# Optimization experiments

Hardware: AMD Instinct MI355X
Metric: run time of the kernel (lower is better)

The kernel has to match this reference:

```python
import jax, jax.numpy as jnp
import numpy as np


def setup_inputs() -> dict:
    key = jax.random.key(0)
    ks = jax.random.split(key, 9)
    B, T, C = 4, 2048, 2048
    E, I, SI = 8, 1408, 5632
    s = lambda k, shape, fan_in: jax.random.normal(k, shape, jnp.float32) * (fan_in ** -0.5)
    return {
        "x": jax.random.normal(ks[0], (B, T, C), jnp.float32),
        "gate_w": s(ks[1], (C, E), C),                  # router: x @ gate_w -> [N,E]
        "expert_gate_w": s(ks[2], (E, C, I), C),        # stacked gate_proj weights
        "expert_up_w": s(ks[3], (E, C, I), C),          # stacked up_proj weights
        "expert_down_w": s(ks[4], (E, I, C), I),        # stacked down_proj weights
        "shared_gate_w": s(ks[5], (C, SI), C),
        "shared_up_w": s(ks[6], (C, SI), C),
        "shared_down_w": s(ks[7], (SI, C), SI),
        "shared_expert_gate_w": s(ks[8], (C, 1), C),
        "top_k": 4,
    }


def reference(x, gate_w, expert_gate_w, expert_up_w, expert_down_w,
              shared_gate_w, shared_up_w, shared_down_w, shared_expert_gate_w, top_k):
    B, T, C = x.shape
    E = gate_w.shape[1]
    xf = x.reshape(-1, C)                      # [N, C]
    N = xf.shape[0]

    # --- router: softmax (fp32) -> top-k -> renormalize ---
    logits = xf @ gate_w                       # [N, E]
    probs = jax.nn.softmax(logits.astype(jnp.float32), axis=-1)
    w, idx = jax.lax.top_k(probs, top_k)       # [N, k]
    w = w / jnp.sum(w, axis=-1, keepdims=True)

    # dense combine gates [N, E]: zero for non-selected experts (equivalent to
    # the torch dispatch/sort/combine: each token gets weight w_k on expert idx_k)
    gates = jnp.zeros((N, E), jnp.float32).at[jnp.arange(N)[:, None], idx].add(w)

    # --- per-expert SwiGLU MLP, accumulated via scan over experts ---
    def step(acc, ew):
        wg, wu, wd, g = ew                     # wg/wu: [C,I], wd: [I,C], g: [N]
        h = jax.nn.silu(xf @ wg) * (xf @ wu)   # [N, I]
        return acc + g[:, None] * (h @ wd), None

    routed, _ = jax.lax.scan(
        step, jnp.zeros_like(xf),
        (expert_gate_w, expert_up_w, expert_down_w, gates.T))

    # --- shared expert with sigmoid gate ---
    shared = (jax.nn.silu(xf @ shared_gate_w) * (xf @ shared_up_w)) @ shared_down_w
    sg = jax.nn.sigmoid(xf @ shared_expert_gate_w)   # [N, 1]

    return (routed + sg * shared).reshape(B, T, C)
```

## Files before the change

kernel.cpp:

```cpp
#include <hip/hip_runtime.h>
#include <hip/hip_bf16.h>
#include <stdint.h>


typedef float f32x4 __attribute__((ext_vector_type(4)));
typedef int   i32x4 __attribute__((ext_vector_type(4)));
typedef __hip_bfloat16 bf16;

#define DEV __device__ __forceinline__

DEV void mfma16(f32x4& c, const i32x4& a, const i32x4& b) {
    asm("v_mfma_f32_16x16x32_bf16 %0, %1, %2, %0" : "+v"(c) : "v"(a), "v"(b));
}

template<int ROWS>
DEV void stage(const bf16* gtile, long ldK, char* lds, int tid) {
    const int wid = tid >> 6, lane = tid & 63;
    const int swz = ((lane & 7) ^ (lane >> 3)) << 4;
    constexpr int NISS = (ROWS * 128) / 4096;
    #pragma unroll
    for (int i = 0; i < NISS; i++) {
        const int o = i * 4096 + wid * 1024;
        const int row = (o >> 7) + (lane >> 3);
        const char* ga = (const char*)gtile + (long)row * (ldK * 2) + swz;
        __builtin_amdgcn_global_load_lds(
            (const __attribute__((address_space(1))) void*)ga,
            (__attribute__((address_space(3))) void*)(lds + o), 16, 0, 0);
    }
}

template<int ROWS>
DEV void stage_idx(const char* base, const long* roff, int ktb, char* lds,
                   int tid, int swz) {
    const int wid = tid >> 6;
    constexpr int NISS = (ROWS * 128) / 4096;
    #pragma unroll
    for (int i = 0; i < NISS; i++) {
        const int o = i * 4096 + wid * 1024;
        const char* ga = base + roff[i] + ktb + swz;
        __builtin_amdgcn_global_load_lds(
            (const __attribute__((address_space(1))) void*)ga,
            (__attribute__((address_space(3))) void*)(lds + o), 16, 0, 0);
    }
}

DEV i32x4 ldsfrag(const char* lds, int row, int kbyte) {
    const int off = (row << 7) + (kbyte ^ ((row & 7) << 4));
    return *(const i32x4*)(lds + off);
}

__global__ __launch_bounds__(256) void tcvt(const float* __restrict__ srcA,
        bf16* __restrict__ dstA, const float* __restrict__ srcB,
        bf16* __restrict__ dstB, int Cd, long dld, long sz, long dz,
        int zsplit) {
    __shared__ float t[64][65];
    long z = blockIdx.z;
    const float* src; bf16* dst;
    if ((int)z < zsplit) { src = srcA; dst = dstA; }
    else { src = srcB; dst = dstB; z -= zsplit; }
    src += z * sz; dst += z * dz;
    const int cb = blockIdx.x * 64, rb = blockIdx.y * 64;
    const int tx = threadIdx.x & 63, ty = threadIdx.x >> 6;
    #pragma unroll
    for (int i = 0; i < 16; i++) {
        const int r = ty + i * 4;
        t[r][tx] = src[(long)(rb + r) * Cd + cb + tx];
    }
    __syncthreads();
    #pragma unroll
    for (int i = 0; i < 16; i++) {
        const int c = ty + i * 4;
        dst[(long)(cb + c) * dld + rb + tx] = __float2bfloat16(t[tx][c]);
    }
}

__global__ __launch_bounds__(256) void cvtx(const float* __restrict__ x,
        bf16* __restrict__ xb, long n4) {
    long i = (long)blockIdx.x * blockDim.x + threadIdx.x;
    const long stride = (long)gridDim.x * blockDim.x;
    for (; i < n4; i += stride) {
        const float4 v = ((const float4*)x)[i];
        union { bf16 h[4]; ushort4 u; } cu;
        cu.h[0] = __float2bfloat16(v.x); cu.h[1] = __float2bfloat16(v.y);
        cu.h[2] = __float2bfloat16(v.z); cu.h[3] = __float2bfloat16(v.w);
        ((ushort4*)xb)[i] = cu.u;
    }
}

__global__ __launch_bounds__(256) void router(const float* __restrict__ x,
        const float* __restrict__ gw, const float* __restrict__ segw,
        int* __restrict__ tidx, float* __restrict__ tw,
        float* __restrict__ sg, int C) {
    const int lane = threadIdx.x & 63;
    const long t = (long)blockIdx.x * 4 + (threadIdx.x >> 6);
    const float* xr = x + t * C;
    float a[9];
    #pragma unroll
    for (int e = 0; e < 9; e++) a[e] = 0.f;
    for (int c = lane; c < C; c += 64) {
        const float xv = xr[c];
        const float4* g4 = (const float4*)(gw + (long)c * 8);
        const float4 g0 = g4[0], g1 = g4[1];
        a[0] += xv * g0.x; a[1] += xv * g0.y; a[2] += xv * g0.z; a[3] += xv * g0.w;
        a[4] += xv * g1.x; a[5] += xv * g1.y; a[6] += xv * g1.z; a[7] += xv * g1.w;
        a[8] += xv * segw[c];
    }
    #pragma unroll
    for (int e = 0; e < 9; e++) {
        #pragma unroll
        for (int o = 32; o; o >>= 1) a[e] += __shfl_xor(a[e], o, 64);
    }
    if (lane == 0) {
        float m = a[0];
        #pragma unroll
        for (int e = 1; e < 8; e++) m = fmaxf(m, a[e]);
        float p[8]; float s = 0.f;
        #pragma unroll
        for (int e = 0; e < 8; e++) { p[e] = expf(a[e] - m); s += p[e]; }
        #pragma unroll
        for (int e = 0; e < 8; e++) p[e] /= s;
        bool used[8] = {false,false,false,false,false,false,false,false};
        float wsum = 0.f; int idx[4]; float wv[4];
        for (int k = 0; k < 4; k++) {
            float best = -1.f; int bi = 0;
            for (int e = 0; e < 8; e++)
                if (!used[e] && p[e] > best) { best = p[e]; bi = e; }
            used[bi] = true; idx[k] = bi; wv[k] = best; wsum += best;
        }
        int4 iv; float4 wv4;
        iv.x = idx[0]; iv.y = idx[1]; iv.z = idx[2]; iv.w = idx[3];
        wv4.x = wv[0] / wsum; wv4.y = wv[1] / wsum;
        wv4.z = wv[2] / wsum; wv4.w = wv[3] / wsum;
        ((int4*)tidx)[t] = iv;
        ((float4*)tw)[t] = wv4;
        sg[t] = 1.f / (1.f + expf(-a[8]));
    }
}

__global__ __launch_bounds__(256) void build_lists(const int* __restrict__ tidx,
        const float* __restrict__ tw, int* __restrict__ tok,
        float* __restrict__ wl, int* __restrict__ cnt, int N) {
    const int e = blockIdx.x;
    const int tid = threadIdx.x;
    const int per = N / 256;
    __shared__ int csum[256];
    int c = 0;
    for (int i = 0; i < per; i++) {
        const int4 id4 = ((const int4*)tidx)[tid * per + i];
        if (id4.x == e || id4.y == e || id4.z == e || id4.w == e) c++;
    }
    csum[tid] = c;
    __syncthreads();
    for (int o = 1; o < 256; o <<= 1) {
        const int v = (tid >= o) ? csum[tid - o] : 0;
        __syncthreads();
        csum[tid] += v;
        __syncthreads();
    }
    int pos = csum[tid] - c;
    if (tid == 255) cnt[e] = csum[255];
    for (int i = 0; i < per; i++) {
        const int t = tid * per + i;
        const int4   id4 = ((const int4*)tidx)[t];
        const float4 w4  = ((const float4*)tw)[t];
        float w = 0.f; int hit = 0;
        if      (id4.x == e) { w = w4.x; hit = 1; }
        else if (id4.y == e) { w = w4.y; hit = 1; }
        else if (id4.z == e) { w = w4.z; hit = 1; }
        else if (id4.w == e) { w = w4.w; hit = 1; }
        if (hit) { tok[(long)e * N + pos] = t; wl[(long)e * N + pos] = w; pos++; }
    }
}

template<int TAG>
__global__ __launch_bounds__(256) void dual_gemm_t(const bf16* __restrict__ A,
        const int* __restrict__ tok, long tokz,
        const int* __restrict__ cnt, int Mfix,
        const bf16* __restrict__ BG0, const bf16* __restrict__ BU0, long bz,
        bf16* __restrict__ H0, long hld, long hz,
        const float* __restrict__ sc0, long scz, int K) {
    __shared__ __align__(128) char Al[16384];
    __shared__ __align__(128) char Gl[8192];
    __shared__ __align__(128) char Ul[8192];
    const int z = blockIdx.z;
    const int Me = cnt ? cnt[z] : Mfix;
    const long m0 = (long)blockIdx.x * 128;
    if (m0 >= Me) return;
    const int* ridx = tok ? tok + (long)z * tokz : nullptr;
    const bf16* BG = BG0 + (long)z * bz;
    const bf16* BU = BU0 + (long)z * bz;
    bf16* H = H0 + (long)z * hz;
    const float* sc = sc0 + (long)z * scz;
    const int tid = threadIdx.x, lane = tid & 63, wid = tid >> 6;
    const long n0 = (long)blockIdx.y * 64;
    const int wm = (wid >> 1) * 64, wn = (wid & 1) * 32;
    const int l15 = lane & 15, lhi = lane >> 4;
    const int swz = ((lane & 7) ^ (lane >> 3)) << 4;
    long roffA[4];
    #pragma unroll
    for (int i = 0; i < 4; i++) {
        const int rit = ((i * 4096 + wid * 1024) >> 7) + (lane >> 3);
        int g = (int)m0 + rit;
        if (ridx) g = ridx[g < Me ? g : Me - 1];
        roffA[i] = (long)g * (K * 2);
    }
    f32x4 ag[4][2] = {}; f32x4 au[4][2] = {};
    for (int kt = 0; kt < K; kt += 64) {
        stage_idx<128>((const char*)A, roffA, kt * 2, Al, tid, swz);
        stage<64>(BG + n0 * K + kt, (long)K, Gl, tid);
        stage<64>(BU + n0 * K + kt, (long)K, Ul, tid);
        __syncthreads();
        #pragma unroll
        for (int ks = 0; ks < 2; ks++) {
            const int kb = ks * 64 + lhi * 16;
            i32x4 af[4], bg[2], bu[2];
            #pragma unroll
            for (int mi = 0; mi < 4; mi++) af[mi] = ldsfrag(Al, wm + mi * 16 + l15, kb);
            #pragma unroll
            for (int ni = 0; ni < 2; ni++) {
                bg[ni] = ldsfrag(Gl, wn + ni * 16 + l15, kb);
                bu[ni] = ldsfrag(Ul, wn + ni * 16 + l15, kb);
            }
            #pragma unroll
            for (int mi = 0; mi < 4; mi++) {
                #pragma unroll
                for (int ni = 0; ni < 2; ni++) {
                    mfma16(ag[mi][ni], af[mi], bg[ni]);
                    mfma16(au[mi][ni], af[mi], bu[ni]);
                }
            }
        }
        __syncthreads();
    }
    asm volatile("s_nop 7\n\ts_nop 7\n\ts_nop 7");
    #pragma unroll
    for (int mi = 0; mi < 4; mi++) {
        #pragma unroll
        for (int r = 0; r < 4; r++) {
            const int pos = (int)m0 + wm + mi * 16 + lhi * 4 + r;
            if (pos < Me) {
                const float s = sc[pos];
                #pragma unroll
                for (int ni = 0; ni < 2; ni++) {
                    const float gv = ag[mi][ni][r], uv = au[mi][ni][r];
                    const float h = (gv / (1.f + expf(-gv))) * uv * s;
                    H[(long)pos * hld + n0 + wn + ni * 16 + l15] = __float2bfloat16(h);
                }
            }
        }
    }
}

template<int TAG>
__global__ __launch_bounds__(256) void gemm_down_t(const bf16* __restrict__ A,
        const bf16* __restrict__ BT, float* __restrict__ C,
        const int* __restrict__ ridx, const int* __restrict__ cntp, int Mfix,
        int K, long ldc, int beta) {
    __shared__ __align__(128) char Al[16384];
    __shared__ __align__(128) char Bl[16384];
    const int Me = cntp ? *cntp : Mfix;
    const long m0 = (long)blockIdx.y * 128;
    if (m0 >= Me) return;
    const int tid = threadIdx.x, lane = tid & 63, wid = tid >> 6;
    const long n0 = (long)blockIdx.x * 128;
    const int wm = (wid >> 1) * 64, wn = (wid & 1) * 64;
    const int l15 = lane & 15, lhi = lane >> 4;
    f32x4 acc[4][4] = {};
    for (int kt = 0; kt < K; kt += 64) {
        stage<128>(A  + m0 * K + kt, (long)K, Al, tid);
        stage<128>(BT + n0 * K + kt, (long)K, Bl, tid);
        __syncthreads();
        #pragma unroll
        for (int ks = 0; ks < 2; ks++) {
            const int kb = ks * 64 + lhi * 16;
            i32x4 af[4], bfr[4];
            #pragma unroll
            for (int mi = 0; mi < 4; mi++) af[mi]  = ldsfrag(Al, wm + mi * 16 + l15, kb);
            #pragma unroll
            for (int ni = 0; ni < 4; ni++) bfr[ni] = ldsfrag(Bl, wn + ni * 16 + l15, kb);
            #pragma unroll
            for (int mi = 0; mi < 4; mi++) {
                #pragma unroll
                for (int ni = 0; ni < 4; ni++) mfma16(acc[mi][ni], af[mi], bfr[ni]);
            }
        }
        __syncthreads();
    }
    asm volatile("s_nop 7\n\ts_nop 7\n\ts_nop 7");
    #pragma unroll
    for (int mi = 0; mi < 4; mi++) {
        #pragma unroll
        for (int r = 0; r < 4; r++) {
            const int pos = (int)m0 + wm + mi * 16 + lhi * 4 + r;
            if (pos < Me) {
                const long orow = ridx ? (long)ridx[pos] : (long)pos;
                #pragma unroll
                for (int ni = 0; ni < 4; ni++) {
                    const long ci = orow * ldc + n0 + wn + ni * 16 + l15;
                    float v = acc[mi][ni][r];
                    if (beta) v += C[ci];
                    C[ci] = v;
                }
            }
        }
    }
}

extern "C" void kernel_launch(void* const* d_in, const int* in_sizes, int n_in,
                              void* d_out, int out_size, void* d_ws, size_t ws_size,
                              hipStream_t stream) {
    const int N = 8192, Cdim = 2048, E = 8, I = 1408, SI = 5632;

    const float* x    = (const float*)d_in[0];
    const float* gw   = (const float*)d_in[1];
    const float* egw  = (const float*)d_in[2];
    const float* euw  = (const float*)d_in[3];
    const float* edw  = (const float*)d_in[4];
    const float* sgw  = (const float*)d_in[5];
    const float* suw  = (const float*)d_in[6];
    const float* sdw  = (const float*)d_in[7];
    const float* segw = (const float*)d_in[8];
    float* out = (float*)d_out;

    char* ws = (char*)d_ws;
    size_t off = 0;
    auto alloc = [&](size_t bytes) { char* p = ws + off; off += (bytes + 255) & ~(size_t)255; return p; };

    bf16*  xb   = (bf16*) alloc((size_t)N * Cdim * 2);
    int*   tidx = (int*)  alloc((size_t)N * 4 * 4);
    float* tw   = (float*)alloc((size_t)N * 4 * 4);
    float* sg   = (float*)alloc((size_t)N * 4);
    int*   tok  = (int*)  alloc((size_t)E * N * 4);
    float* wl   = (float*)alloc((size_t)E * N * 4);
    int*   cnt  = (int*)  alloc(256);
    const size_t commonEnd = off;

    auto planNeed = [&](int EB) {
        const size_t slot = (size_t)(EB * I > SI ? EB * I : SI) * Cdim * 2;
        const size_t h    = (size_t)N * (EB * I > SI ? (size_t)EB * I : (size_t)SI) * 2;
        return commonEnd + 3 * slot + h + 4096;
    };
    const int EB = (ws_size >= planNeed(8)) ? 8 : 4;
    const size_t WSLOT = (size_t)(EB * I > SI ? EB * I : SI) * Cdim * 2;
    const size_t HROWS = (size_t)(EB * I > SI ? (size_t)EB * I : (size_t)SI);
    bf16* Wa = (bf16*)alloc(WSLOT);
    bf16* Wb = (bf16*)alloc(WSLOT);
    bf16* Wc = (bf16*)alloc(WSLOT);
    bf16* Hc = (bf16*)alloc((size_t)N * HROWS * 2);
    if (off > ws_size) return;

    cvtx<<<4096, 256, 0, stream>>>(x, xb, (long)N * Cdim / 4);
    router<<<N / 4, 256, 0, stream>>>(x, gw, segw, tidx, tw, sg, Cdim);
    build_lists<<<E, 256, 0, stream>>>(tidx, tw, tok, wl, cnt, N);

    tcvt<<<dim3(SI / 64, Cdim / 64, 2), 256, 0, stream>>>(
            sgw, Wa, suw, Wb, SI, (long)Cdim, 0, 0, 1);
    tcvt<<<dim3(Cdim / 64, SI / 64, 1), 256, 0, stream>>>(
            sdw, Wc, nullptr, nullptr, Cdim, (long)SI, 0, 0, 1);
    dual_gemm_t<0><<<dim3(N / 128, SI / 64, 1), 256, 0, stream>>>(xb,
            nullptr, 0, nullptr, N, Wa, Wb, 0, Hc, (long)SI, 0, sg, 0, Cdim);
    gemm_down_t<0><<<dim3(Cdim / 128, N / 128), 256, 0, stream>>>(Hc, Wc, out,
            nullptr, nullptr, N, SI, (long)Cdim, 0);

    for (int b = 0; b < E / EB; b++) {
        const int e0 = b * EB;
        tcvt<<<dim3(I / 64, Cdim / 64, 2 * EB), 256, 0, stream>>>(
                egw + (long)e0 * Cdim * I, Wa, euw + (long)e0 * Cdim * I, Wb,
                I, (long)Cdim, (long)Cdim * I, (long)I * Cdim, EB);
        tcvt<<<dim3(Cdim / 64, I / 64, EB), 256, 0, stream>>>(
                edw + (long)e0 * I * Cdim, Wc, nullptr, nullptr,
                Cdim, (long)I, (long)I * Cdim, (long)Cdim * I, EB);

        dual_gemm_t<1><<<dim3(N / 128, I / 64, EB), 256, 0, stream>>>(xb,
                tok + (long)e0 * N, (long)N, cnt + e0, 0,
                Wa, Wb, (long)I * Cdim,
                Hc, (long)I, (long)N * I,
                wl + (long)e0 * N, (long)N, Cdim);

        for (int z = 0; z < EB; z++) {
            gemm_down_t<1><<<dim3(Cdim / 128, N / 128), 256, 0, stream>>>(
                    Hc + (long)z * N * I, Wc + (long)z * Cdim * I, out,
                    tok + (long)(e0 + z) * N, cnt + e0 + z, 0,
                    I, (long)Cdim, 1);
        }
    }
}
```

Before: 1.610 ms.

## Merge shared and routed expert gate/up GEMMs into one launch with compact H

Fuses the x-to-bf16 conversion into the router kernel. Adds a prefix scan over per-expert token counts so the routed hidden activations are stored compactly (4N rows) instead of as N rows per expert. Merges the shared-expert and all routed-expert gate/up GEMMs into one grid launch, so the shared expert fills the tail of the unevenly sized expert work. The aim is fewer launches, less idle GPU time between kernels, less workspace traffic, and a single read of x. The cost is a larger workspace and a heterogeneous grid with branchy per-block setup.

Measured after the change: 1.576 ms. 2.1% less time.

```diff
diff --git a/kernel.cpp b/kernel.cpp
--- a/kernel.cpp
+++ b/kernel.cpp
@@ -74,36 +74,37 @@
     }
 }
 
-__global__ __launch_bounds__(256) void cvtx(const float* __restrict__ x,
-        bf16* __restrict__ xb, long n4) {
-    long i = (long)blockIdx.x * blockDim.x + threadIdx.x;
-    const long stride = (long)gridDim.x * blockDim.x;
-    for (; i < n4; i += stride) {
-        const float4 v = ((const float4*)x)[i];
+__global__ __launch_bounds__(256) void cvtrt(const float* __restrict__ x,
+        const float* __restrict__ gw, const float* __restrict__ segw,
+        bf16* __restrict__ xb, int* __restrict__ tidx, float* __restrict__ tw,
+        float* __restrict__ sg) {
+    const int lane = threadIdx.x & 63;
+    const long t = (long)blockIdx.x * 4 + (threadIdx.x >> 6);
+    const float4* xr = (const float4*)(x + t * 2048);
+    ushort4* xo = (ushort4*)(xb + t * 2048);
+    float a[9];
+    #pragma unroll
+    for (int e = 0; e < 9; e++) a[e] = 0.f;
+    #pragma unroll
+    for (int i = 0; i < 8; i++) {
+        const int c4 = i * 64 + lane;
+        const float4 v = xr[c4];
         union { bf16 h[4]; ushort4 u; } cu;
         cu.h[0] = __float2bfloat16(v.x); cu.h[1] = __float2bfloat16(v.y);
         cu.h[2] = __float2bfloat16(v.z); cu.h[3] = __float2bfloat16(v.w);
-        ((ushort4*)xb)[i] = cu.u;
-    }
-}
-
-__global__ __launch_bounds__(256) void router(const float* __restrict__ x,
-        const float* __restrict__ gw, const float* __restrict__ segw,
-        int* __restrict__ tidx, float* __restrict__ tw,
-        float* __restrict__ sg, int C) {
-    const int lane = threadIdx.x & 63;
-    const long t = (long)blockIdx.x * 4 + (threadIdx.x >> 6);
-    const float* xr = x + t * C;
-    float a[9];
-    #pragma unroll
-    for (int e = 0; e < 9; e++) a[e] = 0.f;
-    for (int c = lane; c < C; c += 64) {
-        const float xv = xr[c];
-        const float4* g4 = (const float4*)(gw + (long)c * 8);
-        const float4 g0 = g4[0], g1 = g4[1];
-        a[0] += xv * g0.x; a[1] += xv * g0.y; a[2] += xv * g0.z; a[3] += xv * g0.w;
-        a[4] += xv * g1.x; a[5] += xv * g1.y; a[6] += xv * g1.z; a[7] += xv * g1.w;
-        a[8] += xv * segw[c];
+        xo[c4] = cu.u;
+        const int c = c4 * 4;
+        const float xv[4] = { v.x, v.y, v.z, v.w };
+        #pragma unroll
+        for (int j = 0; j < 4; j++) {
+            const float4* g4 = (const float4*)(gw + (long)(c + j) * 8);
+            const float4 g0 = g4[0], g1 = g4[1];
+            a[0] += xv[j] * g0.x; a[1] += xv[j] * g0.y;
+            a[2] += xv[j] * g0.z; a[3] += xv[j] * g0.w;
+            a[4] += xv[j] * g1.x; a[5] += xv[j] * g1.y;
+            a[6] += xv[j] * g1.z; a[7] += xv[j] * g1.w;
+            a[8] += xv[j] * segw[c + j];
+        }
     }
     #pragma unroll
     for (int e = 0; e < 9; e++) {
@@ -172,27 +173,43 @@
     }
 }
 
-template<int TAG>
-__global__ __launch_bounds__(256) void dual_gemm_t(const bf16* __restrict__ A,
-        const int* __restrict__ tok, long tokz,
-        const int* __restrict__ cnt, int Mfix,
-        const bf16* __restrict__ BG0, const bf16* __restrict__ BU0, long bz,
-        bf16* __restrict__ H0, long hld, long hz,
-        const float* __restrict__ sc0, long scz, int K) {
+__global__ void scan8(const int* __restrict__ cnt, int* __restrict__ starts) {
+    if (threadIdx.x == 0) {
+        int s = 0;
+        for (int e = 0; e < 8; e++) { starts[e] = s; s += cnt[e]; }
+        starts[8] = s;
+    }
+}
+
+__global__ __launch_bounds__(256) void megadual(const bf16* __restrict__ A0,
+        const int* __restrict__ tok, const int* __restrict__ cnt,
+        const int* __restrict__ starts, int nExpZ, int e0,
+        const bf16* __restrict__ Wea, const bf16* __restrict__ Web, long ebz,
+        const bf16* __restrict__ Wsa, const bf16* __restrict__ Wsb,
+        bf16* __restrict__ He, bf16* __restrict__ Hs,
+        const float* __restrict__ wl, const float* __restrict__ sg, int K) {
     __shared__ __align__(128) char Al[16384];
     __shared__ __align__(128) char Gl[8192];
     __shared__ __align__(128) char Ul[8192];
     const int z = blockIdx.z;
-    const int Me = cnt ? cnt[z] : Mfix;
+    const bf16 *BG, *BU; bf16* H; long hld, n0; const float* sc;
+    const int* ridx; int Me;
+    if (z < nExpZ) {
+        const int e = e0 + z;
+        Me = cnt[e];
+        ridx = tok + (long)e * 8192;
+        BG = Wea + (long)z * ebz; BU = Web + (long)z * ebz;
+        H = He + ((long)starts[e] - starts[e0]) * 1408;
+        hld = 1408; sc = wl + (long)e * 8192;
+        n0 = (long)blockIdx.y * 64;
+    } else {
+        Me = 8192; ridx = nullptr;
+        BG = Wsa; BU = Wsb; H = Hs; hld = 5632; sc = sg;
+        n0 = (long)((z - nExpZ) * gridDim.y + blockIdx.y) * 64;
+    }
     const long m0 = (long)blockIdx.x * 128;
     if (m0 >= Me) return;
-    const int* ridx = tok ? tok + (long)z * tokz : nullptr;
-    const bf16* BG = BG0 + (long)z * bz;
-    const bf16* BU = BU0 + (long)z * bz;
-    bf16* H = H0 + (long)z * hz;
-    const float* sc = sc0 + (long)z * scz;
     const int tid = threadIdx.x, lane = tid & 63, wid = tid >> 6;
-    const long n0 = (long)blockIdx.y * 64;
     const int wm = (wid >> 1) * 64, wn = (wid & 1) * 32;
     const int l15 = lane & 15, lhi = lane >> 4;
     const int swz = ((lane & 7) ^ (lane >> 3)) << 4;
@@ -206,7 +223,7 @@
     }
     f32x4 ag[4][2] = {}; f32x4 au[4][2] = {};
     for (int kt = 0; kt < K; kt += 64) {
-        stage_idx<128>((const char*)A, roffA, kt * 2, Al, tid, swz);
+        stage_idx<128>((const char*)A0, roffA, kt * 2, Al, tid, swz);
         stage<64>(BG + n0 * K + kt, (long)K, Gl, tid);
         stage<64>(BU + n0 * K + kt, (long)K, Ul, tid);
         __syncthreads();
@@ -255,12 +272,14 @@
 __global__ __launch_bounds__(256) void gemm_down_t(const bf16* __restrict__ A,
         const bf16* __restrict__ BT, float* __restrict__ C,
         const int* __restrict__ ridx, const int* __restrict__ cntp, int Mfix,
+        const int* __restrict__ starts, int ia, int ib,
         int K, long ldc, int beta) {
     __shared__ __align__(128) char Al[16384];
     __shared__ __align__(128) char Bl[16384];
     const int Me = cntp ? *cntp : Mfix;
     const long m0 = (long)blockIdx.y * 128;
     if (m0 >= Me) return;
+    if (starts) A += ((long)starts[ia] - starts[ib]) * K;
     const int tid = threadIdx.x, lane = tid & 63, wid = tid >> 6;
     const long n0 = (long)blockIdx.x * 128;
     const int wm = (wid >> 1) * 64, wn = (wid & 1) * 64;
@@ -326,62 +345,97 @@
     size_t off = 0;
     auto alloc = [&](size_t bytes) { char* p = ws + off; off += (bytes + 255) & ~(size_t)255; return p; };
 
-    bf16*  xb   = (bf16*) alloc((size_t)N * Cdim * 2);
-    int*   tidx = (int*)  alloc((size_t)N * 4 * 4);
-    float* tw   = (float*)alloc((size_t)N * 4 * 4);
-    float* sg   = (float*)alloc((size_t)N * 4);
-    int*   tok  = (int*)  alloc((size_t)E * N * 4);
-    float* wl   = (float*)alloc((size_t)E * N * 4);
-    int*   cnt  = (int*)  alloc(256);
+    bf16*  xb     = (bf16*) alloc((size_t)N * Cdim * 2);
+    int*   tidx   = (int*)  alloc((size_t)N * 4 * 4);
+    float* tw     = (float*)alloc((size_t)N * 4 * 4);
+    float* sg     = (float*)alloc((size_t)N * 4);
+    int*   tok    = (int*)  alloc((size_t)E * N * 4);
+    float* wl     = (float*)alloc((size_t)E * N * 4);
+    int*   cnt    = (int*)  alloc(256);
+    int*   starts = (int*)  alloc(256);
     const size_t commonEnd = off;
 
-    auto planNeed = [&](int EB) {
-        const size_t slot = (size_t)(EB * I > SI ? EB * I : SI) * Cdim * 2;
-        const size_t h    = (size_t)N * (EB * I > SI ? (size_t)EB * I : (size_t)SI) * 2;
-        return commonEnd + 3 * slot + h + 4096;
-    };
-    const int EB = (ws_size >= planNeed(8)) ? 8 : 4;
-    const size_t WSLOT = (size_t)(EB * I > SI ? EB * I : SI) * Cdim * 2;
-    const size_t HROWS = (size_t)(EB * I > SI ? (size_t)EB * I : (size_t)SI);
-    bf16* Wa = (bf16*)alloc(WSLOT);
-    bf16* Wb = (bf16*)alloc(WSLOT);
-    bf16* Wc = (bf16*)alloc(WSLOT);
-    bf16* Hc = (bf16*)alloc((size_t)N * HROWS * 2);
+    const size_t EWSLOT = (size_t)E * I * Cdim * 2;
+    const size_t SWSLOT = (size_t)SI * Cdim * 2;
+    const size_t HROWS  = (size_t)4 * N;
+    const size_t mergedNeed = commonEnd + 2 * EWSLOT + 2 * SWSLOT
+                            + (size_t)N * SI * 2 + HROWS * I * 2 + 4096;
+
+    cvtrt<<<N / 4, 256, 0, stream>>>(x, gw, segw, xb, tidx, tw, sg);
+    build_lists<<<E, 256, 0, stream>>>(tidx, tw, tok, wl, cnt, N);
+    scan8<<<1, 64, 0, stream>>>(cnt, starts);
+
+    if (ws_size >= mergedNeed) {
+        bf16* Wea = (bf16*)alloc(EWSLOT);
+        bf16* Web = (bf16*)alloc(EWSLOT);
+        bf16* Wsa = (bf16*)alloc(SWSLOT);
+        bf16* Wsb = (bf16*)alloc(SWSLOT);
+        bf16* Hs  = (bf16*)alloc((size_t)N * SI * 2);
+        bf16* He  = (bf16*)alloc(HROWS * I * 2);
+        bf16* Wsc = Wea;
+        bf16* Wec = Web;
+
+        tcvt<<<dim3(SI / 64, Cdim / 64, 2), 256, 0, stream>>>(
+                sgw, Wsa, suw, Wsb, SI, (long)Cdim, 0, 0, 1);
+        tcvt<<<dim3(I / 64, Cdim / 64, 2 * E), 256, 0, stream>>>(
+                egw, Wea, euw, Web, I, (long)Cdim,
+                (long)Cdim * I, (long)I * Cdim, E);
+
+        megadual<<<dim3(N / 128, I / 64, E + 4), 256, 0, stream>>>(xb,
+                tok, cnt, starts, E, 0, Wea, Web, (long)I * Cdim,
+                Wsa, Wsb, He, Hs, wl, sg, Cdim);
+
+        tcvt<<<dim3(Cdim / 64, SI / 64, 1), 256, 0, stream>>>(
+                sdw, Wsc, nullptr, nullptr, Cdim, (long)SI, 0, 0, 1);
+        tcvt<<<dim3(Cdim / 64, I / 64, E), 256, 0, stream>>>(
+                edw, Wec, nullptr, nullptr, Cdim, (long)I,
+                (long)I * Cdim, (long)Cdim * I, E);
+
+        gemm_down_t<0><<<dim3(Cdim / 128, N / 128), 256, 0, stream>>>(
+                Hs, Wsc, out, nullptr, nullptr, N, nullptr, 0, 0,
+                SI, (long)Cdim, 0);
+        for (int e = 0; e < E; e++) {
+            gemm_down_t<1><<<dim3(Cdim / 128, N / 128), 256, 0, stream>>>(
+                    He, Wec + (long)e * Cdim * I, out,
+                    tok + (long)e * N, cnt + e, 0, starts, e, 0,
+                    I, (long)Cdim, 1);
+        }
+        return;
+    }
+
+    bf16* Wa = (bf16*)alloc(SWSLOT);
+    bf16* Wb = (bf16*)alloc(SWSLOT);
+    bf16* Wc = (bf16*)alloc(SWSLOT);
+    bf16* Hs = (bf16*)alloc((size_t)N * SI * 2);
+    bf16* He = (bf16*)alloc(HROWS * I * 2);
     if (off > ws_size) return;
-
-    cvtx<<<4096, 256, 0, stream>>>(x, xb, (long)N * Cdim / 4);
-    router<<<N / 4, 256, 0, stream>>>(x, gw, segw, tidx, tw, sg, Cdim);
-    build_lists<<<E, 256, 0, stream>>>(tidx, tw, tok, wl, cnt, N);
 
     tcvt<<<dim3(SI / 64, Cdim / 64, 2), 256, 0, stream>>>(
             sgw, Wa, suw, Wb, SI, (long)Cdim, 0, 0, 1);
     tcvt<<<dim3(Cdim / 64, SI / 64, 1), 256, 0, stream>>>(
             sdw, Wc, nullptr, nullptr, Cdim, (long)SI, 0, 0, 1);
-    dual_gemm_t<0><<<dim3(N / 128, SI / 64, 1), 256, 0, stream>>>(xb,
-            nullptr, 0, nullptr, N, Wa, Wb, 0, Hc, (long)SI, 0, sg, 0, Cdim);
-    gemm_down_t<0><<<dim3(Cdim / 128, N / 128), 256, 0, stream>>>(Hc, Wc, out,
-            nullptr, nullptr, N, SI, (long)Cdim, 0);
-
-    for (int b = 0; b < E / EB; b++) {
-        const int e0 = b * EB;
-        tcvt<<<dim3(I / 64, Cdim / 64, 2 * EB), 256, 0, stream>>>(
+    megadual<<<dim3(N / 128, I / 64, 4), 256, 0, stream>>>(xb,
+            tok, cnt, starts, 0, 0, nullptr, nullptr, 0,
+            Wa, Wb, nullptr, Hs, wl, sg, Cdim);
+    gemm_down_t<0><<<dim3(Cdim / 128, N / 128), 256, 0, stream>>>(
+            Hs, Wc, out, nullptr, nullptr, N, nullptr, 0, 0, SI, (long)Cdim, 0);
+
+    for (int b = 0; b < 2; b++) {
+        const int e0 = b * 4;
+        tcvt<<<dim3(I / 64, Cdim / 64, 8), 256, 0, stream>>>(
                 egw + (long)e0 * Cdim * I, Wa, euw + (long)e0 * Cdim * I, Wb,
-                I, (long)Cdim, (long)Cdim * I, (long)I * Cdim, EB);
-        tcvt<<<dim3(Cdim / 64, I / 64, EB), 256, 0, stream>>>(
+                I, (long)Cdim, (long)Cdim * I, (long)I * Cdim, 4);
+        megadual<<<dim3(N / 128, I / 64, 4), 256, 0, stream>>>(xb,
+                tok, cnt, starts, 4, e0, Wa, Wb, (long)I * Cdim,
+                nullptr, nullptr, He, nullptr, wl, sg, Cdim);
+        tcvt<<<dim3(Cdim / 64, I / 64, 4), 256, 0, stream>>>(
                 edw + (long)e0 * I * Cdim, Wc, nullptr, nullptr,
-                Cdim, (long)I, (long)I * Cdim, (long)Cdim * I, EB);
-
-        dual_gemm_t<1><<<dim3(N / 128, I / 64, EB), 256, 0, stream>>>(xb,
-                tok + (long)e0 * N, (long)N, cnt + e0, 0,
-                Wa, Wb, (long)I * Cdim,
-                Hc, (long)I, (long)N * I,
-                wl + (long)e0 * N, (long)N, Cdim);
-
-        for (int z = 0; z < EB; z++) {
+                Cdim, (long)I, (long)I * Cdim, (long)Cdim * I, 4);
+        for (int z = 0; z < 4; z++) {
             gemm_down_t<1><<<dim3(Cdim / 128, N / 128), 256, 0, stream>>>(
-                    Hc + (long)z * N * I, Wc + (long)z * Cdim * I, out,
+                    He, Wc + (long)z * Cdim * I, out,
                     tok + (long)(e0 + z) * N, cnt + e0 + z, 0,
-                    I, (long)Cdim, 1);
-        }
-    }
-}
+                    starts, e0 + z, e0, I, (long)Cdim, 1);
+        }
+    }
+}
```
